# Kernel optimization log

Measured on AMD Instinct MI355X. Metric: run time of the kernel, lower is better.

## Reference

```python
import jax, jax.numpy as jnp
import numpy as np
from jax import lax

B, F, H, W = 1, 8, 16, 16
DIM, HEADS, HD, RANK, T = 1920, 30, 64, 128, 226
SV = F * H * W          # 2048 video tokens
S = T + SV              # 2274 total tokens


def setup_inputs() -> dict:
    key = jax.random.key(0)
    ks = jax.random.split(key, 12)
    r = lambda k, sh, s: jax.random.normal(k, sh, dtype=jnp.float32) * s
    theta = jax.random.uniform(ks[0], (SV, HD), dtype=jnp.float32) * (2.0 * np.pi)
    return dict(
        hidden_states=r(ks[1], (B, SV, DIM), 1.0),
        encoder_hidden_states=r(ks[2], (B, T, DIM), 1.0),
        cos=jnp.cos(theta),
        sin=jnp.sin(theta),
        to_q_w=r(ks[3], (DIM, DIM), 0.02), to_q_b=r(ks[4], (DIM,), 0.02),
        to_k_w=r(ks[5], (DIM, DIM), 0.02), to_k_b=r(ks[6], (DIM,), 0.02),
        to_v_w=r(ks[7], (DIM, DIM), 0.02), to_v_b=r(ks[8], (DIM,), 0.02),
        norm_q_w=jnp.ones((HD,), jnp.float32), norm_q_b=jnp.zeros((HD,), jnp.float32),
        norm_k_w=jnp.ones((HD,), jnp.float32), norm_k_b=jnp.zeros((HD,), jnp.float32),
        conv1_w=r(ks[9], (RANK, DIM, 3), 0.05),
        conv2_w=r(ks[10], (DIM, RANK, 3), 0.05),
        to_out_w=r(ks[11], (DIM, DIM), 0.02),
        to_out_b=jnp.zeros((DIM,), jnp.float32),
    )


def _layernorm(x, w, b, eps=1e-6):
    mu = jnp.mean(x, axis=-1, keepdims=True)
    var = jnp.mean(jnp.square(x - mu), axis=-1, keepdims=True)
    return (x - mu) * lax.rsqrt(var + eps) * w + b


def _rope(x, cos, sin):
    # diffusers interleaved RoPE: pairs (even, odd) along last dim
    xr, xi = x[..., 0::2], x[..., 1::2]
    x_rot = jnp.stack([-xi, xr], axis=-1).reshape(x.shape)
    return x * cos + x_rot * sin


def _conv1d(x, w):  # x: [N, C, L], w: [O, I, K], SAME padding
    return lax.conv_general_dilated(x, w, window_strides=(1,), padding=((1, 1),),
                                    dimension_numbers=('NCH', 'OIH', 'NCH'))


def reference(hidden_states, encoder_hidden_states, cos, sin,
              to_q_w, to_q_b, to_k_w, to_k_b, to_v_w, to_v_b,
              norm_q_w, norm_q_b, norm_k_w, norm_k_b,
              conv1_w, conv2_w, to_out_w, to_out_b):
    # --- temporal conv1d side branch on video tokens only ---
    x = hidden_states.reshape(B, F, H, W, DIM)
    x = jnp.transpose(x, (0, 2, 3, 4, 1)).reshape(B * H * W, DIM, F)  # [BHW, C, F]
    x = _conv1d(x, conv1_w)
    x = jax.nn.gelu(x, approximate=False)
    x = _conv1d(x, conv2_w)
    x = x.reshape(B, H, W, DIM, F)
    conv_branch = jnp.transpose(x, (0, 4, 1, 2, 3)).reshape(B, SV, DIM)

    # --- joint text+video attention ---
    hs = jnp.concatenate([encoder_hidden_states, hidden_states], axis=1)  # [B, S, D]
    q = hs @ to_q_w.T + to_q_b
    k = hs @ to_k_w.T + to_k_b
    v = hs @ to_v_w.T + to_v_b
    q = q.reshape(B, S, HEADS, HD).transpose(0, 2, 1, 3)  # [B, Hh, S, hd]
    k = k.reshape(B, S, HEADS, HD).transpose(0, 2, 1, 3)
    v = v.reshape(B, S, HEADS, HD).transpose(0, 2, 1, 3)

    q = _layernorm(q, norm_q_w, norm_q_b)
    k = _layernorm(k, norm_k_w, norm_k_b)

    # partial RoPE: only video portion (tokens past text_seq_length)
    q = jnp.concatenate([q[:, :, :T], _rope(q[:, :, T:], cos, sin)], axis=2)
    k = jnp.concatenate([k[:, :, :T], _rope(k[:, :, T:], cos, sin)], axis=2)

    scale = 1.0 / np.sqrt(HD).astype(np.float32)
    scores = jnp.einsum('bhqd,bhkd->bhqk', q, k) * scale
    probs = jax.nn.softmax(scores, axis=-1)
    out = jnp.einsum('bhqk,bhkd->bhqd', probs, v)
    out = out.transpose(0, 2, 1, 3).reshape(B, S, DIM)

    # residual add of conv branch into video slice
    out = jnp.concatenate([out[:, :T], out[:, T:] + conv_branch], axis=1)
    out = out @ to_out_w.T + to_out_b

    return out[:, T:], out[:, :T]  # (hidden_states, encoder_hidden_states)
```

## Files before the change

### kernel.cpp

```cpp
#include <hip/hip_runtime.h>
#include <hip/hip_bf16.h>
#include <math.h>

#define F_     8
#define DIM_   1920
#define HEADS_ 30
#define HD_    64
#define RANK_  128
#define T_     226
#define SV_    2048
#define S_     2274

#define BM 128
#define BN 128
#define BK 32

using short8  = __attribute__((ext_vector_type(8))) short;
using f32x4   = __attribute__((ext_vector_type(4))) float;
using i32x4v  = __attribute__((ext_vector_type(4))) int;
using ushort4v= __attribute__((ext_vector_type(4))) unsigned short;

__device__ __forceinline__ unsigned short f2b(float f) {
  unsigned int u = __float_as_uint(f);
  u = (u + 0x7FFFu + ((u >> 16) & 1u)) >> 16;
  return (unsigned short)u;
}
__device__ __forceinline__ float b2f(unsigned short s) {
  return __uint_as_float(((unsigned int)s) << 16);
}
__device__ __forceinline__ void gload_lds16(const void* g, void* l) {
  __builtin_amdgcn_global_load_lds(
      (const __attribute__((address_space(1))) unsigned int*)g,
      (__attribute__((address_space(3))) unsigned int*)l, 16, 0, 0);
}
__device__ __forceinline__ void xcd_swz(int& bx, int& by) {
  const int nx = gridDim.x;
  const int nwg = nx * gridDim.y;
  const int lid = by * nx + bx;
  const int q = nwg >> 3, r = nwg & 7;
  const int xcd = lid & 7, pos = lid >> 3;
  const int wg = (xcd < r ? xcd * (q + 1) : r * (q + 1) + (xcd - r) * q) + pos;
  bx = wg % nx; by = wg / nx;
}

template<int AMODE, int OUTMODE>
__global__ __launch_bounds__(256) void gemm_mfma(
    const unsigned short* __restrict__ A,
    const unsigned short* __restrict__ A2,
    const unsigned short* __restrict__ B,
    const float* __restrict__ bias,
    void* __restrict__ Cout,
    int M, int N, int K, int lda, int ldb, int kinner)
{
  __shared__ __align__(16) unsigned short As[BM * BK];
  __shared__ __align__(16) unsigned short Bs[BN * BK];
  if constexpr (AMODE == 3) {
    const int z = blockIdx.z;
    A += (size_t)z * 480;
    B += (size_t)(z >> 2) * 256 * DIM_ + (z & 3) * 480;
    Cout = (void*)((float*)Cout + (size_t)z * M * N);
  }
  int bx = blockIdx.x, by = blockIdx.y;
  xcd_swz(bx, by);
  const int t   = threadIdx.x;
  const int w   = t >> 6, l = t & 63;
  const int wr  = w >> 1, wc = w & 1;
  const int row0 = by * BM, col0 = bx * BN;
  const int lr  = l & 15;
  const int lcg = l >> 4;
  const int sel = (lr >> 1) & 3;
  const int sr  = t >> 2;
  const int sc  = t & 3;

  f32x4 acc[4][4];
#pragma unroll
  for (int i = 0; i < 4; ++i)
#pragma unroll
    for (int j = 0; j < 4; ++j) acc[i][j] = (f32x4){0.f, 0.f, 0.f, 0.f};

  for (int k0 = 0; k0 < K; k0 += BK) {
    int kseg = 0, kcol = k0;
    if constexpr (AMODE == 1) { kseg = k0 / kinner; kcol = k0 - kseg * kinner; }
#pragma unroll
    for (int it = 0; it < 2; ++it) {
      const int r    = it * 64 + sr;
      const int csrc = sc ^ ((r >> 1) & 3);
      int ar = row0 + r; if (ar > M - 1) ar = M - 1;
      const unsigned short* asrc;
      if constexpr (AMODE == 1) {
        asrc = A + (size_t)(ar + kseg * 256) * kinner + kcol + csrc * 8;
      } else if constexpr (AMODE == 2) {
        asrc = (ar < T_) ? (A  + (size_t)ar        * DIM_ + k0 + csrc * 8)
                         : (A2 + (size_t)(ar - T_) * DIM_ + k0 + csrc * 8);
      } else {
        asrc = A + (size_t)ar * lda + k0 + csrc * 8;
      }
      gload_lds16(asrc, (char*)As + it * 4096 + t * 16);
      const unsigned short* bsrc = B + (size_t)(col0 + r) * ldb + k0 + csrc * 8;
      gload_lds16(bsrc, (char*)Bs + it * 4096 + t * 16);
    }
    __syncthreads();

    short8 af[4], bfv[4];
#pragma unroll
    for (int m = 0; m < 4; ++m) {
      int r = wr * 64 + m * 16 + lr;
      af[m] = *(const short8*)((const char*)As + r * 64 + ((lcg ^ sel) << 4));
    }
#pragma unroll
    for (int n = 0; n < 4; ++n) {
      int r = wc * 64 + n * 16 + lr;
      bfv[n] = *(const short8*)((const char*)Bs + r * 64 + ((lcg ^ sel) << 4));
    }
    __builtin_amdgcn_s_setprio(1);
#pragma unroll
    for (int m = 0; m < 4; ++m)
#pragma unroll
      for (int n = 0; n < 4; ++n)
        acc[m][n] = __builtin_amdgcn_mfma_f32_16x16x32_bf16(af[m], bfv[n], acc[m][n], 0, 0, 0);
    __builtin_amdgcn_s_setprio(0);
    __syncthreads();
  }

#pragma unroll
  for (int m = 0; m < 4; ++m) {
    const int rbase = row0 + wr * 64 + m * 16 + lcg * 4;
#pragma unroll
    for (int n = 0; n < 4; ++n) {
      const int c = col0 + wc * 64 + n * 16 + lr;
      const float bi = bias ? bias[c] : 0.f;
#pragma unroll
      for (int reg = 0; reg < 4; ++reg) {
        const int r = rbase + reg;
        if (r >= M) continue;
        const float v = acc[m][n][reg] + bi;
        if constexpr (OUTMODE == 0) {
          ((float*)Cout)[(size_t)r * N + c] = v;
        } else if constexpr (OUTMODE == 1) {
          ((unsigned short*)Cout)[(size_t)r * N + c] = f2b(v);
        } else if constexpr (OUTMODE == 2) {
          const size_t orow = (r >= T_) ? (size_t)(r - T_) : (size_t)(SV_ + r);
          ((float*)Cout)[orow * N + c] = v;
        } else {
          const int buf = c / DIM_, cc = c - buf * DIM_;
          ((unsigned short*)Cout)[(size_t)buf * S_ * DIM_ + (size_t)r * DIM_ + cc] = f2b(v);
        }
      }
    }
  }
}

__global__ __launch_bounds__(256) void attn_mfma(
    const unsigned short* __restrict__ Qbb,
    const unsigned short* __restrict__ Kbb,
    const unsigned short* __restrict__ Vbb,
    unsigned short* __restrict__ Op0,
    unsigned short* __restrict__ Op1,
    float* __restrict__ ml)
{
  __shared__ __align__(16) unsigned short Kl[2][64 * 64];
  __shared__ __align__(16) unsigned short Vt[2][64 * 64];

  const int sv = blockIdx.z;
  int bx = blockIdx.x, by = blockIdx.y;
  xcd_swz(bx, by);
  const int qb = bx, h = by;
  const int t = threadIdx.x, w = t >> 6, l = t & 63;
  const int lr = l & 15, lg = l >> 4;
  const int q0 = qb * 64;
  const int j0base = sv * 1152;
  const int NT = 18;
  unsigned short* Opart = sv ? Op1 : Op0;

  short8 qa[2];
  {
    int qrow = q0 + w * 16 + lr; if (qrow >= S_) qrow = S_ - 1;
    const unsigned short* qp = Qbb + (size_t)qrow * DIM_ + h * 64 + lg * 8;
    qa[0] = *(const short8*)qp;
    qa[1] = *(const short8*)(qp + 32);
  }

  const int krow0 = t >> 3;
  const int kc0 = ((((t & 7) * 16) ^ ((krow0        & 7) << 4)) >> 1);
  const int kc1 = ((((t & 7) * 16) ^ (((krow0 + 32) & 7) << 4)) >> 1);

  f32x4 oacc[4];
#pragma unroll
  for (int n = 0; n < 4; ++n) oacc[n] = (f32x4){0.f, 0.f, 0.f, 0.f};
  float m_run = -1e30f, l_run = 0.f;

  const int addrA = (lr + ((lg & 1) << 5)) << 2;
  const bool hi_m = (lg & 2) != 0;

  {
    int k0 = j0base + krow0;      if (k0 >= S_) k0 = S_ - 1;
    int k1 = j0base + krow0 + 32; if (k1 >= S_) k1 = S_ - 1;
    gload_lds16(Kbb + (size_t)k0 * DIM_ + h * 64 + kc0, (char*)Kl[0] + t * 16);
    gload_lds16(Kbb + (size_t)k1 * DIM_ + h * 64 + kc1, (char*)Kl[0] + 4096 + t * 16);
    int key = j0base + l; if (key >= S_) key = S_ - 1;
    const unsigned short* vp = Vbb + (size_t)key * DIM_ + h * 64 + w * 16;
    short8 v0 = *(const short8*)vp;
    short8 v1 = *(const short8*)(vp + 8);
#pragma unroll
    for (int i = 0; i < 8; ++i)
      Vt[0][(w * 16 + i) * 64 + (l ^ ((i & 7) << 3))] = (unsigned short)v0[i];
#pragma unroll
    for (int i = 8; i < 16; ++i)
      Vt[0][(w * 16 + i) * 64 + (l ^ ((i & 7) << 3))] = (unsigned short)v1[i - 8];
  }
  __syncthreads();

  for (int jt = 0; jt < NT; ++jt) {
    const int j0 = j0base + jt * 64;
    const int cur = jt & 1;

    const int jn0 = (jt + 1 < NT) ? j0 + 64 : j0;
    {
      int k0 = jn0 + krow0;      if (k0 >= S_) k0 = S_ - 1;
      int k1 = jn0 + krow0 + 32; if (k1 >= S_) k1 = S_ - 1;
      gload_lds16(Kbb + (size_t)k0 * DIM_ + h * 64 + kc0,
                  (char*)Kl[cur ^ 1] + t * 16);
      gload_lds16(Kbb + (size_t)k1 * DIM_ + h * 64 + kc1,
                  (char*)Kl[cur ^ 1] + 4096 + t * 16);
    }
    short8 nv0, nv1;
    {
      int key = jn0 + l; if (key >= S_) key = S_ - 1;
      const unsigned short* vp = Vbb + (size_t)key * DIM_ + h * 64 + w * 16;
      nv0 = *(const short8*)vp;
      nv1 = *(const short8*)(vp + 8);
    }

    f32x4 sacc[4];
#pragma unroll
    for (int m = 0; m < 4; ++m) sacc[m] = (f32x4){0.f, 0.f, 0.f, 0.f};
    __builtin_amdgcn_s_setprio(1);
#pragma unroll
    for (int m = 0; m < 4; ++m) {
#pragma unroll
      for (int ks = 0; ks < 2; ++ks) {
        const short8 kb = *(const short8*)((const char*)Kl[cur] + (m * 16 + lr) * 128 +
                              ((ks * 64 + lg * 16) ^ ((lr & 7) << 4)));
        sacc[m] = __builtin_amdgcn_mfma_f32_16x16x32_bf16(kb, qa[ks], sacc[m], 0, 0, 0);
      }
    }
    __builtin_amdgcn_s_setprio(0);
    if (j0 + 64 > S_) {
#pragma unroll
      for (int m = 0; m < 4; ++m)
#pragma unroll
        for (int r = 0; r < 4; ++r)
          if (j0 + m * 16 + lg * 4 + r >= S_) sacc[m][r] = -1e30f;
    }

    float mx = sacc[0][0];
#pragma unroll
    for (int m = 0; m < 4; ++m)
#pragma unroll
      for (int r = 0; r < 4; ++r) mx = fmaxf(mx, sacc[m][r]);
    mx = fmaxf(mx, __shfl_xor(mx, 16));
    mx = fmaxf(mx, __shfl_xor(mx, 32));

    if (!__all(mx <= m_run + 8.0f)) {
      const float mnew = fmaxf(m_run, mx);
      const float sc = exp2f(m_run - mnew);
      l_run *= sc;
      float scr[4];
#pragma unroll
      for (int r = 0; r < 4; ++r) scr[r] = __shfl(sc, (l & 48) | (lg * 4 + r));
#pragma unroll
      for (int n = 0; n < 4; ++n)
#pragma unroll
        for (int r = 0; r < 4; ++r) oacc[n][r] *= scr[r];
      m_run = mnew;
    }

    float rs = 0.f;
    int c[4][2];
#pragma unroll
    for (int m = 0; m < 4; ++m) {
      const float p0 = exp2f(sacc[m][0] - m_run);
      const float p1 = exp2f(sacc[m][1] - m_run);
      const float p2 = exp2f(sacc[m][2] - m_run);
      const float p3 = exp2f(sacc[m][3] - m_run);
      rs += (p0 + p1) + (p2 + p3);
      asm("v_cvt_pk_bf16_f32 %0, %1, %2" : "=v"(c[m][0]) : "v"(p0), "v"(p1));
      asm("v_cvt_pk_bf16_f32 %0, %1, %2" : "=v"(c[m][1]) : "v"(p2), "v"(p3));
    }
    rs += __shfl_xor(rs, 16);
    rs += __shfl_xor(rs, 32);
    l_run += rs;

    __builtin_amdgcn_s_setprio(1);
#pragma unroll
    for (int ks = 0; ks < 2; ++ks) {
      const int a0 = __builtin_amdgcn_ds_bpermute(addrA,      c[2 * ks][0]);
      const int b0 = __builtin_amdgcn_ds_bpermute(addrA,      c[2 * ks + 1][0]);
      const int a1 = __builtin_amdgcn_ds_bpermute(addrA,      c[2 * ks][1]);
      const int b1 = __builtin_amdgcn_ds_bpermute(addrA,      c[2 * ks + 1][1]);
      const int a2 = __builtin_amdgcn_ds_bpermute(addrA + 64, c[2 * ks][0]);
      const int b2 = __builtin_amdgcn_ds_bpermute(addrA + 64, c[2 * ks + 1][0]);
      const int a3 = __builtin_amdgcn_ds_bpermute(addrA + 64, c[2 * ks][1]);
      const int b3 = __builtin_amdgcn_ds_bpermute(addrA + 64, c[2 * ks + 1][1]);
      i32x4v pw;
      pw[0] = hi_m ? b0 : a0;
      pw[1] = hi_m ? b1 : a1;
      pw[2] = hi_m ? b2 : a2;
      pw[3] = hi_m ? b3 : a3;
      const short8 pa = __builtin_bit_cast(short8, pw);
#pragma unroll
      for (int n = 0; n < 4; ++n) {
        const short8 vb = *(const short8*)((const char*)Vt[cur] + (n * 16 + lr) * 128 +
                              ((ks * 64 + lg * 16) ^ ((lr & 7) << 4)));
        oacc[n] = __builtin_amdgcn_mfma_f32_16x16x32_bf16(pa, vb, oacc[n], 0, 0, 0);
      }
    }
    __builtin_amdgcn_s_setprio(0);

#pragma unroll
    for (int i = 0; i < 8; ++i)
      Vt[cur ^ 1][(w * 16 + i) * 64 + (l ^ ((i & 7) << 3))] = (unsigned short)nv0[i];
#pragma unroll
    for (int i = 8; i < 16; ++i)
      Vt[cur ^ 1][(w * 16 + i) * 64 + (l ^ ((i & 7) << 3))] = (unsigned short)nv1[i - 8];
    __syncthreads();
  }

#pragma unroll
  for (int r = 0; r < 4; ++r) {
    const int row = q0 + w * 16 + lg * 4 + r;
    if (row >= S_) continue;
#pragma unroll
    for (int n = 0; n < 4; ++n)
      Opart[(size_t)row * DIM_ + h * 64 + n * 16 + lr] = f2b(oacc[n][r]);
  }
  if (l < 16) {
    const int row = q0 + w * 16 + lr;
    if (row < S_) {
      float2 v; v.x = m_run; v.y = l_run;
      *(float2*)(ml + ((size_t)(sv * S_ + row) * HEADS_ + h) * 2) = v;
    }
  }
}

__global__ void merge_k(const unsigned short* __restrict__ Op0,
                        const unsigned short* __restrict__ Op1,
                        const float* __restrict__ ml,
                        const unsigned short* __restrict__ y2b,
                        unsigned short* __restrict__ dst)
{
  const int i = blockIdx.x * 256 + threadIdx.x;
  if (i >= S_ * DIM_ / 8) return;
  const int e = i * 8;
  const int row = e / DIM_, col = e % DIM_;
  const int h = col >> 6;
  const float* p0 = ml + ((size_t)row * HEADS_ + h) * 2;
  const float* p1 = ml + ((size_t)(S_ + row) * HEADS_ + h) * 2;
  const float m0 = p0[0], l0 = p0[1], m1 = p1[0], l1 = p1[1];
  const float M = fmaxf(m0, m1);
  const float w0 = exp2f(m0 - M), w1 = exp2f(m1 - M);
  const float inv = 1.f / (w0 * l0 + w1 * l1);
  const short8 a = *(const short8*)(Op0 + e);
  const short8 b = *(const short8*)(Op1 + e);
  const bool cadd = row >= T_;
  const unsigned short* yp = y2b + (size_t)(row - T_) * DIM_ + col;
  short8 o;
#pragma unroll
  for (int j = 0; j < 8; ++j) {
    float v = (w0 * b2f((unsigned short)a[j]) + w1 * b2f((unsigned short)b[j])) * inv;
    if (cadd) v += b2f(yp[j]);
    o[j] = (short)f2b(v);
  }
  *(short8*)(dst + e) = o;
}

#define U0_ 1228800
#define U1_ 3993600
#define U2_ 4427520
#define U3_ 5164800
#define U4_ 5902080
#define U5_ 5907840
__global__ void prep_all(const float* __restrict__ hid, const float* __restrict__ enc,
                         const float* __restrict__ w1, const float* __restrict__ w2,
                         const float* __restrict__ qw, const float* __restrict__ kw,
                         const float* __restrict__ vw, const float* __restrict__ qb2,
                         const float* __restrict__ kb2, const float* __restrict__ vb2,
                         unsigned short* __restrict__ hidpad, unsigned short* __restrict__ encb,
                         unsigned short* __restrict__ w1p, unsigned short* __restrict__ w2p,
                         unsigned short* __restrict__ wqkv, float* __restrict__ bqkv)
{
  const int i = blockIdx.x * 256 + threadIdx.x;
  if (i < U0_) {
    const int e = i * 4;
    const int r = e / DIM_;
    ushort4v o = (ushort4v){0, 0, 0, 0};
    if (r >= 256 && r < 256 + SV_) {
      const float4 v = *(const float4*)(hid + e - 256 * DIM_);
      o[0] = f2b(v.x); o[1] = f2b(v.y); o[2] = f2b(v.z); o[3] = f2b(v.w);
    }
    *(ushort4v*)(hidpad + e) = o;
  } else if (i < U1_) {
    const int e = (i - U0_) * 4;
    const int which = e / (DIM_ * DIM_);
    const int j = e - which * DIM_ * DIM_;
    const float* s = which == 0 ? qw : which == 1 ? kw : vw;
    const float4 v = *(const float4*)(s + j);
    ushort4v o = {f2b(v.x), f2b(v.y), f2b(v.z), f2b(v.w)};
    *(ushort4v*)(wqkv + e) = o;
  } else if (i < U2_) {
    const int e = i - U1_;
    encb[e] = f2b(enc[e]);
  } else if (i < U3_) {
    const int e = i - U2_;
    const int oc = e / (DIM_ * 3), rem = e % (DIM_ * 3);
    const int ks = rem / DIM_, ic = rem % DIM_;
    w1p[e] = f2b(w1[(size_t)oc * DIM_ * 3 + ic * 3 + ks]);
  } else if (i < U4_) {
    const int e = i - U3_;
    const int oc = e / (RANK_ * 3), rem = e % (RANK_ * 3);
    const int ks = rem / RANK_, rc = rem % RANK_;
    w2p[e] = f2b(w2[(size_t)oc * RANK_ * 3 + rc * 3 + ks]);
  } else if (i < U5_) {
    const int e = i - U4_;
    const int which = e / DIM_, j = e % DIM_;
    bqkv[e] = which == 0 ? qb2[j] : which == 1 ? kb2[j] : vb2[j];
  }
}

__global__ void cvt_w(const float* __restrict__ src, unsigned short* __restrict__ dst, int n)
{
  int i = blockIdx.x * 256 + threadIdx.x;
  if (i < n) dst[i] = f2b(src[i]);
}

__global__ void gelupad_k(const float* __restrict__ y1T, unsigned short* __restrict__ dst)
{
  int i = blockIdx.x * 256 + threadIdx.x;
  if (i >= 2560 * RANK_) return;
  int r = i / RANK_, rc = i % RANK_;
  unsigned short o = 0;
  if (r >= 256 && r < 256 + SV_) {
    int s = r - 256;
    float x = 0.f;
#pragma unroll
    for (int z = 0; z < 12; ++z)
      x += y1T[(size_t)z * RANK_ * SV_ + (size_t)rc * SV_ + s];
    o = f2b(0.5f * x * (1.f + erff(x * 0.70710678118654752f)));
  }
  dst[i] = o;
}

__global__ __launch_bounds__(256) void qknorm_rope(
    unsigned short* __restrict__ Qbb, unsigned short* __restrict__ Kbb,
    const float* __restrict__ nq_w, const float* __restrict__ nq_b,
    const float* __restrict__ nk_w, const float* __restrict__ nk_b,
    const float* __restrict__ cosT, const float* __restrict__ sinT)
{
  const int w = threadIdx.x >> 6, lane = threadIdx.x & 63;
  const int idx = blockIdx.x * 4 + w;
  if (idx >= S_ * HEADS_) return;
  const int s = idx / HEADS_, h = idx % HEADS_;
  unsigned short* X = blockIdx.y ? Kbb : Qbb;
  const float* wt = blockIdx.y ? nk_w : nq_w;
  const float* bt = blockIdx.y ? nk_b : nq_b;
  const size_t off = (size_t)s * DIM_ + h * HD_ + lane;
  float x = b2f(X[off]);
  float m = x;
#pragma unroll
  for (int o = 32; o; o >>= 1) m += __shfl_xor(m, o);
  m *= (1.f / 64.f);
  float d = x - m;
  float v = d * d;
#pragma unroll
  for (int o = 32; o; o >>= 1) v += __shfl_xor(v, o);
  v *= (1.f / 64.f);
  float y = d * rsqrtf(v + 1e-6f) * wt[lane] + bt[lane];
  if (s >= T_) {
    float p = __shfl_xor(y, 1);
    float rot = (lane & 1) ? p : -p;
    int sv = s - T_;
    y = y * cosT[(size_t)sv * HD_ + lane] + rot * sinT[(size_t)sv * HD_ + lane];
  }
  if (!blockIdx.y) y *= 0.18033688011112042f;
  X[off] = f2b(y);
}

extern "C" void kernel_launch(void* const* d_in, const int* in_sizes, int n_in,
                              void* d_out, int out_size, void* d_ws, size_t ws_size,
                              hipStream_t stream)
{
  const float* hidden  = (const float*)d_in[0];
  const float* encoder = (const float*)d_in[1];
  const float* cosT    = (const float*)d_in[2];
  const float* sinT    = (const float*)d_in[3];
  const float* to_q_w  = (const float*)d_in[4];
  const float* to_q_b  = (const float*)d_in[5];
  const float* to_k_w  = (const float*)d_in[6];
  const float* to_k_b  = (const float*)d_in[7];
  const float* to_v_w  = (const float*)d_in[8];
  const float* to_v_b  = (const float*)d_in[9];
  const float* nq_w    = (const float*)d_in[10];
  const float* nq_b    = (const float*)d_in[11];
  const float* nk_w    = (const float*)d_in[12];
  const float* nk_b    = (const float*)d_in[13];
  const float* conv1_w = (const float*)d_in[14];
  const float* conv2_w = (const float*)d_in[15];
  const float* to_out_w = (const float*)d_in[16];
  const float* to_out_b = (const float*)d_in[17];
  float* out = (float*)d_out;

  char* p = (char*)d_ws;
  unsigned short* hidpad = (unsigned short*)p;  p += (size_t)2560 * DIM_ * 2;
  unsigned short* y2b    = (unsigned short*)p;  p += (size_t)SV_ * DIM_ * 2;
  unsigned short* wqkv   = (unsigned short*)p;  p += (size_t)3 * DIM_ * DIM_ * 2;
  unsigned short* w1p    = (unsigned short*)p;  p += (size_t)RANK_ * DIM_ * 3 * 2;
  unsigned short* w2p    = (unsigned short*)p;  p += (size_t)DIM_ * RANK_ * 3 * 2;
  unsigned short* QKVbb  = (unsigned short*)p;  p += (size_t)3 * S_ * DIM_ * 2;
  unsigned short* encb   = (unsigned short*)p;  p += (size_t)T_ * DIM_ * 2;
  float*          y1T    = (float*)p;           p += (size_t)12 * RANK_ * SV_ * 4;
  unsigned short* gelup  = (unsigned short*)p;  p += (size_t)2560 * RANK_ * 2;
  float*          bqkv   = (float*)p;           p += (size_t)3 * DIM_ * 4;
  unsigned short* Qbb = QKVbb;
  unsigned short* Kbb = QKVbb + (size_t)S_ * DIM_;
  unsigned short* Vbb = QKVbb + (size_t)2 * S_ * DIM_;
  unsigned short* Op0 = hidpad;
  unsigned short* Op1 = (unsigned short*)y1T;
  float*          ml  = (float*)((char*)y1T + (size_t)S_ * DIM_ * 2);

  prep_all<<<(U5_ + 255) / 256, 256, 0, stream>>>(
      hidden, encoder, conv1_w, conv2_w, to_q_w, to_k_w, to_v_w,
      to_q_b, to_k_b, to_v_b, hidpad, encb, w1p, w2p, wqkv, bqkv);

  gemm_mfma<3, 0><<<dim3(SV_ / BN, 1, 12), 256, 0, stream>>>(
      w1p, nullptr, hidpad, nullptr, y1T, RANK_, SV_, 480, DIM_ * 3, DIM_, 1);
  gelupad_k<<<(2560 * RANK_ + 255) / 256, 256, 0, stream>>>(y1T, gelup);
  gemm_mfma<1, 1><<<dim3(DIM_ / BN, SV_ / BM), 256, 0, stream>>>(
      gelup, nullptr, w2p, nullptr, y2b, SV_, DIM_, RANK_ * 3, RANK_ * 3, RANK_ * 3, RANK_);

  const unsigned short* hid0 = hidpad + (size_t)256 * DIM_;
  gemm_mfma<2, 3><<<dim3(3 * DIM_ / BN, (S_ + BM - 1) / BM), 256, 0, stream>>>(
      encb, hid0, wqkv, bqkv, QKVbb, S_, 3 * DIM_, DIM_, DIM_, DIM_, 1);

  qknorm_rope<<<dim3((S_ * HEADS_ + 3) / 4, 2), 256, 0, stream>>>(
      Qbb, Kbb, nq_w, nq_b, nk_w, nk_b, cosT, sinT);

  attn_mfma<<<dim3((S_ + 63) / 64, HEADS_, 2), 256, 0, stream>>>(
      Qbb, Kbb, Vbb, Op0, Op1, ml);

  merge_k<<<(S_ * DIM_ / 8 + 255) / 256, 256, 0, stream>>>(Op0, Op1, ml, y2b, Qbb);

  cvt_w<<<(DIM_ * DIM_ + 255) / 256, 256, 0, stream>>>(to_out_w, wqkv, DIM_ * DIM_);
  gemm_mfma<0, 2><<<dim3(DIM_ / BN, (S_ + BM - 1) / BM), 256, 0, stream>>>(
      Qbb, nullptr, wqkv, to_out_b, out, S_, DIM_, DIM_, DIM_, DIM_, 1);
}
```

Measured before the change: 406.2 us.

## Process two query tiles per wave in attention and fuse out-weight cast into merge

Each attention wave now handles 32 query rows as two 16-row sub-tiles that share every K and V tile loaded from shared memory. This halves the grid, the K/V global and LDS traffic per query, and the loop overhead. The to_out weight bf16 conversion is folded into the merge kernel with vectorised loads, removing one launch. The trade-offs are more registers per thread, possibly lower occupancy, and fewer blocks (18×30×2) to fill the GPU.

```diff
diff --git a/kernel.cpp b/kernel.cpp
--- a/kernel.cpp
+++ b/kernel.cpp
@@ -150,6 +150,24 @@
   }
 }
 
+__device__ __forceinline__ short8 build_pa(int c0lo, int c0hi, int c1lo, int c1hi,
+                                           int addrA, bool hi_m) {
+  const int a0 = __builtin_amdgcn_ds_bpermute(addrA,      c0lo);
+  const int b0 = __builtin_amdgcn_ds_bpermute(addrA,      c1lo);
+  const int a1 = __builtin_amdgcn_ds_bpermute(addrA,      c0hi);
+  const int b1 = __builtin_amdgcn_ds_bpermute(addrA,      c1hi);
+  const int a2 = __builtin_amdgcn_ds_bpermute(addrA + 64, c0lo);
+  const int b2 = __builtin_amdgcn_ds_bpermute(addrA + 64, c1lo);
+  const int a3 = __builtin_amdgcn_ds_bpermute(addrA + 64, c0hi);
+  const int b3 = __builtin_amdgcn_ds_bpermute(addrA + 64, c1hi);
+  i32x4v pw;
+  pw[0] = hi_m ? b0 : a0;
+  pw[1] = hi_m ? b1 : a1;
+  pw[2] = hi_m ? b2 : a2;
+  pw[3] = hi_m ? b3 : a3;
+  return __builtin_bit_cast(short8, pw);
+}
+
 __global__ __launch_bounds__(256) void attn_mfma(
     const unsigned short* __restrict__ Qbb,
     const unsigned short* __restrict__ Kbb,
@@ -167,27 +185,32 @@
   const int qb = bx, h = by;
   const int t = threadIdx.x, w = t >> 6, l = t & 63;
   const int lr = l & 15, lg = l >> 4;
-  const int q0 = qb * 64;
+  const int q0 = qb * 128;
   const int j0base = sv * 1152;
   const int NT = 18;
   unsigned short* Opart = sv ? Op1 : Op0;
 
-  short8 qa[2];
+  short8 qaA[2], qaB[2];
   {
-    int qrow = q0 + w * 16 + lr; if (qrow >= S_) qrow = S_ - 1;
-    const unsigned short* qp = Qbb + (size_t)qrow * DIM_ + h * 64 + lg * 8;
-    qa[0] = *(const short8*)qp;
-    qa[1] = *(const short8*)(qp + 32);
+    int qrA = q0 + w * 32 + lr;      if (qrA >= S_) qrA = S_ - 1;
+    int qrB = q0 + w * 32 + 16 + lr; if (qrB >= S_) qrB = S_ - 1;
+    const unsigned short* qpA = Qbb + (size_t)qrA * DIM_ + h * 64 + lg * 8;
+    const unsigned short* qpB = Qbb + (size_t)qrB * DIM_ + h * 64 + lg * 8;
+    qaA[0] = *(const short8*)qpA; qaA[1] = *(const short8*)(qpA + 32);
+    qaB[0] = *(const short8*)qpB; qaB[1] = *(const short8*)(qpB + 32);
   }
 
   const int krow0 = t >> 3;
   const int kc0 = ((((t & 7) * 16) ^ ((krow0        & 7) << 4)) >> 1);
   const int kc1 = ((((t & 7) * 16) ^ (((krow0 + 32) & 7) << 4)) >> 1);
 
-  f32x4 oacc[4];
-#pragma unroll
-  for (int n = 0; n < 4; ++n) oacc[n] = (f32x4){0.f, 0.f, 0.f, 0.f};
-  float m_run = -1e30f, l_run = 0.f;
+  f32x4 oaccA[4], oaccB[4];
+#pragma unroll
+  for (int n = 0; n < 4; ++n) {
+    oaccA[n] = (f32x4){0.f, 0.f, 0.f, 0.f};
+    oaccB[n] = (f32x4){0.f, 0.f, 0.f, 0.f};
+  }
+  float mA = -1e30f, lA = 0.f, mB = -1e30f, lB = 0.f;
 
   const int addrA = (lr + ((lg & 1) << 5)) << 2;
   const bool hi_m = (lg & 2) != 0;
@@ -231,9 +254,9 @@
       nv1 = *(const short8*)(vp + 8);
     }
 
-    f32x4 sacc[4];
-#pragma unroll
-    for (int m = 0; m < 4; ++m) sacc[m] = (f32x4){0.f, 0.f, 0.f, 0.f};
+    f32x4 sA[4], sB[4];
+#pragma unroll
+    for (int m = 0; m < 4; ++m) { sA[m] = (f32x4){0.f,0.f,0.f,0.f}; sB[m] = (f32x4){0.f,0.f,0.f,0.f}; }
     __builtin_amdgcn_s_setprio(1);
 #pragma unroll
     for (int m = 0; m < 4; ++m) {
@@ -241,7 +264,8 @@
       for (int ks = 0; ks < 2; ++ks) {
         const short8 kb = *(const short8*)((const char*)Kl[cur] + (m * 16 + lr) * 128 +
                               ((ks * 64 + lg * 16) ^ ((lr & 7) << 4)));
-        sacc[m] = __builtin_amdgcn_mfma_f32_16x16x32_bf16(kb, qa[ks], sacc[m], 0, 0, 0);
+        sA[m] = __builtin_amdgcn_mfma_f32_16x16x32_bf16(kb, qaA[ks], sA[m], 0, 0, 0);
+        sB[m] = __builtin_amdgcn_mfma_f32_16x16x32_bf16(kb, qaB[ks], sB[m], 0, 0, 0);
       }
     }
     __builtin_amdgcn_s_setprio(0);
@@ -250,69 +274,65 @@
       for (int m = 0; m < 4; ++m)
 #pragma unroll
         for (int r = 0; r < 4; ++r)
-          if (j0 + m * 16 + lg * 4 + r >= S_) sacc[m][r] = -1e30f;
-    }
-
-    float mx = sacc[0][0];
+          if (j0 + m * 16 + lg * 4 + r >= S_) { sA[m][r] = -1e30f; sB[m][r] = -1e30f; }
+    }
+
+    float mxA = sA[0][0], mxB = sB[0][0];
 #pragma unroll
     for (int m = 0; m < 4; ++m)
 #pragma unroll
-      for (int r = 0; r < 4; ++r) mx = fmaxf(mx, sacc[m][r]);
-    mx = fmaxf(mx, __shfl_xor(mx, 16));
-    mx = fmaxf(mx, __shfl_xor(mx, 32));
-
-    if (!__all(mx <= m_run + 8.0f)) {
-      const float mnew = fmaxf(m_run, mx);
-      const float sc = exp2f(m_run - mnew);
-      l_run *= sc;
-      float scr[4];
-#pragma unroll
-      for (int r = 0; r < 4; ++r) scr[r] = __shfl(sc, (l & 48) | (lg * 4 + r));
+      for (int r = 0; r < 4; ++r) { mxA = fmaxf(mxA, sA[m][r]); mxB = fmaxf(mxB, sB[m][r]); }
+    mxA = fmaxf(mxA, __shfl_xor(mxA, 16));
+    mxA = fmaxf(mxA, __shfl_xor(mxA, 32));
+    mxB = fmaxf(mxB, __shfl_xor(mxB, 16));
+    mxB = fmaxf(mxB, __shfl_xor(mxB, 32));
+
+    if (!__all(mxA <= mA + 8.0f && mxB <= mB + 8.0f)) {
+      const float mnA = fmaxf(mA, mxA), mnB = fmaxf(mB, mxB);
+      const float scA = exp2f(mA - mnA), scB = exp2f(mB - mnB);
+      lA *= scA; lB *= scB;
+      float srA[4], srB[4];
+#pragma unroll
+      for (int r = 0; r < 4; ++r) {
+        srA[r] = __shfl(scA, (l & 48) | (lg * 4 + r));
+        srB[r] = __shfl(scB, (l & 48) | (lg * 4 + r));
+      }
 #pragma unroll
       for (int n = 0; n < 4; ++n)
 #pragma unroll
-        for (int r = 0; r < 4; ++r) oacc[n][r] *= scr[r];
-      m_run = mnew;
-    }
-
-    float rs = 0.f;
-    int c[4][2];
+        for (int r = 0; r < 4; ++r) { oaccA[n][r] *= srA[r]; oaccB[n][r] *= srB[r]; }
+      mA = mnA; mB = mnB;
+    }
+
+    float rsA = 0.f, rsB = 0.f;
+    int cA[4][2], cB[4][2];
 #pragma unroll
     for (int m = 0; m < 4; ++m) {
-      const float p0 = exp2f(sacc[m][0] - m_run);
-      const float p1 = exp2f(sacc[m][1] - m_run);
-      const float p2 = exp2f(sacc[m][2] - m_run);
-      const float p3 = exp2f(sacc[m][3] - m_run);
-      rs += (p0 + p1) + (p2 + p3);
-      asm("v_cvt_pk_bf16_f32 %0, %1, %2" : "=v"(c[m][0]) : "v"(p0), "v"(p1));
-      asm("v_cvt_pk_bf16_f32 %0, %1, %2" : "=v"(c[m][1]) : "v"(p2), "v"(p3));
-    }
-    rs += __shfl_xor(rs, 16);
-    rs += __shfl_xor(rs, 32);
-    l_run += rs;
+      const float a0 = exp2f(sA[m][0] - mA), a1 = exp2f(sA[m][1] - mA);
+      const float a2 = exp2f(sA[m][2] - mA), a3 = exp2f(sA[m][3] - mA);
+      rsA += (a0 + a1) + (a2 + a3);
+      asm("v_cvt_pk_bf16_f32 %0, %1, %2" : "=v"(cA[m][0]) : "v"(a0), "v"(a1));
+      asm("v_cvt_pk_bf16_f32 %0, %1, %2" : "=v"(cA[m][1]) : "v"(a2), "v"(a3));
+      const float b0 = exp2f(sB[m][0] - mB), b1 = exp2f(sB[m][1] - mB);
+      const float b2 = exp2f(sB[m][2] - mB), b3 = exp2f(sB[m][3] - mB);
+      rsB += (b0 + b1) + (b2 + b3);
+      asm("v_cvt_pk_bf16_f32 %0, %1, %2" : "=v"(cB[m][0]) : "v"(b0), "v"(b1));
+      asm("v_cvt_pk_bf16_f32 %0, %1, %2" : "=v"(cB[m][1]) : "v"(b2), "v"(b3));
+    }
+    rsA += __shfl_xor(rsA, 16); rsA += __shfl_xor(rsA, 32); lA += rsA;
+    rsB += __shfl_xor(rsB, 16); rsB += __shfl_xor(rsB, 32); lB += rsB;
 
     __builtin_amdgcn_s_setprio(1);
 #pragma unroll
     for (int ks = 0; ks < 2; ++ks) {
-      const int a0 = __builtin_amdgcn_ds_bpermute(addrA,      c[2 * ks][0]);
-      const int b0 = __builtin_amdgcn_ds_bpermute(addrA,      c[2 * ks + 1][0]);
-      const int a1 = __builtin_amdgcn_ds_bpermute(addrA,      c[2 * ks][1]);
-      const int b1 = __builtin_amdgcn_ds_bpermute(addrA,      c[2 * ks + 1][1]);
-      const int a2 = __builtin_amdgcn_ds_bpermute(addrA + 64, c[2 * ks][0]);
-      const int b2 = __builtin_amdgcn_ds_bpermute(addrA + 64, c[2 * ks + 1][0]);
-      const int a3 = __builtin_amdgcn_ds_bpermute(addrA + 64, c[2 * ks][1]);
-      const int b3 = __builtin_amdgcn_ds_bpermute(addrA + 64, c[2 * ks + 1][1]);
-      i32x4v pw;
-      pw[0] = hi_m ? b0 : a0;
-      pw[1] = hi_m ? b1 : a1;
-      pw[2] = hi_m ? b2 : a2;
-      pw[3] = hi_m ? b3 : a3;
-      const short8 pa = __builtin_bit_cast(short8, pw);
+      const short8 paA = build_pa(cA[2*ks][0], cA[2*ks][1], cA[2*ks+1][0], cA[2*ks+1][1], addrA, hi_m);
+      const short8 paB = build_pa(cB[2*ks][0], cB[2*ks][1], cB[2*ks+1][0], cB[2*ks+1][1], addrA, hi_m);
 #pragma unroll
       for (int n = 0; n < 4; ++n) {
         const short8 vb = *(const short8*)((const char*)Vt[cur] + (n * 16 + lr) * 128 +
                               ((ks * 64 + lg * 16) ^ ((lr & 7) << 4)));
-        oacc[n] = __builtin_amdgcn_mfma_f32_16x16x32_bf16(pa, vb, oacc[n], 0, 0, 0);
+        oaccA[n] = __builtin_amdgcn_mfma_f32_16x16x32_bf16(paA, vb, oaccA[n], 0, 0, 0);
+        oaccB[n] = __builtin_amdgcn_mfma_f32_16x16x32_bf16(paB, vb, oaccB[n], 0, 0, 0);
       }
     }
     __builtin_amdgcn_s_setprio(0);
@@ -328,50 +348,75 @@
 
 #pragma unroll
   for (int r = 0; r < 4; ++r) {
-    const int row = q0 + w * 16 + lg * 4 + r;
-    if (row >= S_) continue;
-#pragma unroll
-    for (int n = 0; n < 4; ++n)
-      Opart[(size_t)row * DIM_ + h * 64 + n * 16 + lr] = f2b(oacc[n][r]);
+    const int rowA = q0 + w * 32 + lg * 4 + r;
+    const int rowB = rowA + 16;
+    if (rowA < S_) {
+#pragma unroll
+      for (int n = 0; n < 4; ++n)
+        Opart[(size_t)rowA * DIM_ + h * 64 + n * 16 + lr] = f2b(oaccA[n][r]);
+    }
+    if (rowB < S_) {
+#pragma unroll
+      for (int n = 0; n < 4; ++n)
+        Opart[(size_t)rowB * DIM_ + h * 64 + n * 16 + lr] = f2b(oaccB[n][r]);
+    }
   }
   if (l < 16) {
-    const int row = q0 + w * 16 + lr;
-    if (row < S_) {
-      float2 v; v.x = m_run; v.y = l_run;
-      *(float2*)(ml + ((size_t)(sv * S_ + row) * HEADS_ + h) * 2) = v;
-    }
-  }
-}
-
+    const int rowA = q0 + w * 32 + lr;
+    const int rowB = rowA + 16;
+    if (rowA < S_) {
+      float2 v; v.x = mA; v.y = lA;
+      *(float2*)(ml + ((size_t)(sv * S_ + rowA) * HEADS_ + h) * 2) = v;
+    }
+    if (rowB < S_) {
+      float2 v; v.x = mB; v.y = lB;
+      *(float2*)(ml + ((size_t)(sv * S_ + rowB) * HEADS_ + h) * 2) = v;
+    }
+  }
+}
+
+#define MERGE_N_ (S_ * DIM_ / 8)
+#define CVT_N_   (DIM_ * DIM_ / 8)
 __global__ void merge_k(const unsigned short* __restrict__ Op0,
                         const unsigned short* __restrict__ Op1,
                         const float* __restrict__ ml,
                         const unsigned short* __restrict__ y2b,
-                        unsigned short* __restrict__ dst)
+                        unsigned short* __restrict__ dst,
+                        const float* __restrict__ ow,
+                        unsigned short* __restrict__ owb)
 {
   const int i = blockIdx.x * 256 + threadIdx.x;
-  if (i >= S_ * DIM_ / 8) return;
-  const int e = i * 8;
-  const int row = e / DIM_, col = e % DIM_;
-  const int h = col >> 6;
-  const float* p0 = ml + ((size_t)row * HEADS_ + h) * 2;
-  const float* p1 = ml + ((size_t)(S_ + row) * HEADS_ + h) * 2;
-  const float m0 = p0[0], l0 = p0[1], m1 = p1[0], l1 = p1[1];
-  const float M = fmaxf(m0, m1);
-  const float w0 = exp2f(m0 - M), w1 = exp2f(m1 - M);
-  const float inv = 1.f / (w0 * l0 + w1 * l1);
-  const short8 a = *(const short8*)(Op0 + e);
-  const short8 b = *(const short8*)(Op1 + e);
-  const bool cadd = row >= T_;
-  const unsigned short* yp = y2b + (size_t)(row - T_) * DIM_ + col;
-  short8 o;
-#pragma unroll
-  for (int j = 0; j < 8; ++j) {
-    float v = (w0 * b2f((unsigned short)a[j]) + w1 * b2f((unsigned short)b[j])) * inv;
-    if (cadd) v += b2f(yp[j]);
-    o[j] = (short)f2b(v);
-  }
-  *(short8*)(dst + e) = o;
+  if (i < MERGE_N_) {
+    const int e = i * 8;
+    const int row = e / DIM_, col = e % DIM_;
+    const int h = col >> 6;
+    const float* p0 = ml + ((size_t)row * HEADS_ + h) * 2;
+    const float* p1 = ml + ((size_t)(S_ + row) * HEADS_ + h) * 2;
+    const float m0 = p0[0], l0 = p0[1], m1 = p1[0], l1 = p1[1];
+    const float M = fmaxf(m0, m1);
+    const float w0 = exp2f(m0 - M), w1 = exp2f(m1 - M);
+    const float inv = 1.f / (w0 * l0 + w1 * l1);
+    const short8 a = *(const short8*)(Op0 + e);
+    const short8 b = *(const short8*)(Op1 + e);
+    const bool cadd = row >= T_;
+    const unsigned short* yp = y2b + (size_t)(row - T_) * DIM_ + col;
+    short8 o;
+#pragma unroll
+    for (int j = 0; j < 8; ++j) {
+      float v = (w0 * b2f((unsigned short)a[j]) + w1 * b2f((unsigned short)b[j])) * inv;
+      if (cadd) v += b2f(yp[j]);
+      o[j] = (short)f2b(v);
+    }
+    *(short8*)(dst + e) = o;
+  } else if (i < MERGE_N_ + CVT_N_) {
+    const int e = (i - MERGE_N_) * 8;
+    const float4 v0 = *(const float4*)(ow + e);
+    const float4 v1 = *(const float4*)(ow + e + 4);
+    short8 o;
+    o[0]=(short)f2b(v0.x); o[1]=(short)f2b(v0.y); o[2]=(short)f2b(v0.z); o[3]=(short)f2b(v0.w);
+    o[4]=(short)f2b(v1.x); o[5]=(short)f2b(v1.y); o[6]=(short)f2b(v1.z); o[7]=(short)f2b(v1.w);
+    *(short8*)(owb + e) = o;
+  }
 }
 
 #define U0_ 1228800
@@ -427,12 +472,6 @@
   }
 }
 
-__global__ void cvt_w(const float* __restrict__ src, unsigned short* __restrict__ dst, int n)
-{
-  int i = blockIdx.x * 256 + threadIdx.x;
-  if (i < n) dst[i] = f2b(src[i]);
-}
-
 __global__ void gelupad_k(const float* __restrict__ y1T, unsigned short* __restrict__ dst)
 {
   int i = blockIdx.x * 256 + threadIdx.x;
@@ -544,12 +583,12 @@
   qknorm_rope<<<dim3((S_ * HEADS_ + 3) / 4, 2), 256, 0, stream>>>(
       Qbb, Kbb, nq_w, nq_b, nk_w, nk_b, cosT, sinT);
 
-  attn_mfma<<<dim3((S_ + 63) / 64, HEADS_, 2), 256, 0, stream>>>(
+  attn_mfma<<<dim3((S_ + 127) / 128, HEADS_, 2), 256, 0, stream>>>(
       Qbb, Kbb, Vbb, Op0, Op1, ml);
 
-  merge_k<<<(S_ * DIM_ / 8 + 255) / 256, 256, 0, stream>>>(Op0, Op1, ml, y2b, Qbb);
-
-  cvt_w<<<(DIM_ * DIM_ + 255) / 256, 256, 0, stream>>>(to_out_w, wqkv, DIM_ * DIM_);
+  merge_k<<<(MERGE_N_ + CVT_N_ + 255) / 256, 256, 0, stream>>>(
+      Op0, Op1, ml, y2b, Qbb, to_out_w, wqkv);
+
   gemm_mfma<0, 2><<<dim3(DIM_ / BN, (S_ + BM - 1) / BM), 256, 0, stream>>>(
       Qbb, nullptr, wqkv, to_out_b, out, S_, DIM_, DIM_, DIM_, DIM_, 1);
 }
```

Result: slower. 420.2 us (+3.4%).

## Write V transposed from QKV GEMM and feed attention PV directly from global

Applied to the files above, without the earlier changes.

The QKV projection epilogue now writes the V third as a transposed [DIM, padded-S] bf16 buffer using 4-wide stores. The attention kernel then loads V^T fragments straight into registers, split across the QK^T phase. This removes the per-tile LDS transpose, its scalar shared-memory writes and half the LDS footprint. Separately, the to_out weight conversion is folded into the merge kernel with vectorized loads, saving one launch. The trade-offs are strided, less-coalesced GEMM epilogue stores and global-latency V reads inside the attention loop. The padding columns of V^T are never initialized, so stale or NaN values there could leak into the output even though the matching probabilities are zero.

```diff
diff --git a/kernel.cpp b/kernel.cpp
--- a/kernel.cpp
+++ b/kernel.cpp
@@ -10,6 +10,7 @@
 #define T_     226
 #define SV_    2048
 #define S_     2274
+#define SP_    2304
 
 #define BM 128
 #define BN 128
@@ -50,6 +51,7 @@
     const unsigned short* __restrict__ B,
     const float* __restrict__ bias,
     void* __restrict__ Cout,
+    unsigned short* __restrict__ VT,
     int M, int N, int K, int lda, int ldb, int kinner)
 {
   __shared__ __align__(16) unsigned short As[BM * BK];
@@ -129,37 +131,75 @@
     for (int n = 0; n < 4; ++n) {
       const int c = col0 + wc * 64 + n * 16 + lr;
       const float bi = bias ? bias[c] : 0.f;
-#pragma unroll
-      for (int reg = 0; reg < 4; ++reg) {
-        const int r = rbase + reg;
-        if (r >= M) continue;
-        const float v = acc[m][n][reg] + bi;
-        if constexpr (OUTMODE == 0) {
-          ((float*)Cout)[(size_t)r * N + c] = v;
-        } else if constexpr (OUTMODE == 1) {
-          ((unsigned short*)Cout)[(size_t)r * N + c] = f2b(v);
-        } else if constexpr (OUTMODE == 2) {
-          const size_t orow = (r >= T_) ? (size_t)(r - T_) : (size_t)(SV_ + r);
-          ((float*)Cout)[orow * N + c] = v;
+      if constexpr (OUTMODE == 3) {
+        const int buf = c / DIM_, cc = c - buf * DIM_;
+        if (buf == 2) {
+          unsigned short* vt = VT + (size_t)cc * SP_ + rbase;
+          if (rbase + 4 <= M) {
+            ushort4v o = {f2b(acc[m][n][0] + bi), f2b(acc[m][n][1] + bi),
+                          f2b(acc[m][n][2] + bi), f2b(acc[m][n][3] + bi)};
+            *(ushort4v*)vt = o;
+          } else {
+#pragma unroll
+            for (int reg = 0; reg < 4; ++reg)
+              if (rbase + reg < M) vt[reg] = f2b(acc[m][n][reg] + bi);
+          }
         } else {
-          const int buf = c / DIM_, cc = c - buf * DIM_;
-          ((unsigned short*)Cout)[(size_t)buf * S_ * DIM_ + (size_t)r * DIM_ + cc] = f2b(v);
+#pragma unroll
+          for (int reg = 0; reg < 4; ++reg) {
+            const int r = rbase + reg;
+            if (r < M)
+              ((unsigned short*)Cout)[(size_t)buf * S_ * DIM_ + (size_t)r * DIM_ + cc]
+                  = f2b(acc[m][n][reg] + bi);
+          }
+        }
+      } else {
+#pragma unroll
+        for (int reg = 0; reg < 4; ++reg) {
+          const int r = rbase + reg;
+          if (r >= M) continue;
+          const float v = acc[m][n][reg] + bi;
+          if constexpr (OUTMODE == 0) {
+            ((float*)Cout)[(size_t)r * N + c] = v;
+          } else if constexpr (OUTMODE == 1) {
+            ((unsigned short*)Cout)[(size_t)r * N + c] = f2b(v);
+          } else {
+            const size_t orow = (r >= T_) ? (size_t)(r - T_) : (size_t)(SV_ + r);
+            ((float*)Cout)[orow * N + c] = v;
+          }
         }
       }
     }
   }
+}
+
+__device__ __forceinline__ short8 build_pa(int c0lo, int c0hi, int c1lo, int c1hi,
+                                           int addrA, bool hi_m) {
+  const int a0 = __builtin_amdgcn_ds_bpermute(addrA,      c0lo);
+  const int b0 = __builtin_amdgcn_ds_bpermute(addrA,      c1lo);
+  const int a1 = __builtin_amdgcn_ds_bpermute(addrA,      c0hi);
+  const int b1 = __builtin_amdgcn_ds_bpermute(addrA,      c1hi);
+  const int a2 = __builtin_amdgcn_ds_bpermute(addrA + 64, c0lo);
+  const int b2 = __builtin_amdgcn_ds_bpermute(addrA + 64, c1lo);
+  const int a3 = __builtin_amdgcn_ds_bpermute(addrA + 64, c0hi);
+  const int b3 = __builtin_amdgcn_ds_bpermute(addrA + 64, c1hi);
+  i32x4v pw;
+  pw[0] = hi_m ? b0 : a0;
+  pw[1] = hi_m ? b1 : a1;
+  pw[2] = hi_m ? b2 : a2;
+  pw[3] = hi_m ? b3 : a3;
+  return __builtin_bit_cast(short8, pw);
 }
 
 __global__ __launch_bounds__(256) void attn_mfma(
     const unsigned short* __restrict__ Qbb,
     const unsigned short* __restrict__ Kbb,
-    const unsigned short* __restrict__ Vbb,
+    const unsigned short* __restrict__ VT,
     unsigned short* __restrict__ Op0,
     unsigned short* __restrict__ Op1,
     float* __restrict__ ml)
 {
   __shared__ __align__(16) unsigned short Kl[2][64 * 64];
-  __shared__ __align__(16) unsigned short Vt[2][64 * 64];
 
   const int sv = blockIdx.z;
   int bx = blockIdx.x, by = blockIdx.y;
@@ -179,6 +219,7 @@
     qa[0] = *(const short8*)qp;
     qa[1] = *(const short8*)(qp + 32);
   }
+  const unsigned short* vtb = VT + (size_t)(h * 64 + lr) * SP_ + lg * 8;
 
   const int krow0 = t >> 3;
   const int kc0 = ((((t & 7) * 16) ^ ((krow0        & 7) << 4)) >> 1);
@@ -197,16 +238,6 @@
     int k1 = j0base + krow0 + 32; if (k1 >= S_) k1 = S_ - 1;
     gload_lds16(Kbb + (size_t)k0 * DIM_ + h * 64 + kc0, (char*)Kl[0] + t * 16);
     gload_lds16(Kbb + (size_t)k1 * DIM_ + h * 64 + kc1, (char*)Kl[0] + 4096 + t * 16);
-    int key = j0base + l; if (key >= S_) key = S_ - 1;
-    const unsigned short* vp = Vbb + (size_t)key * DIM_ + h * 64 + w * 16;
-    short8 v0 = *(const short8*)vp;
-    short8 v1 = *(const short8*)(vp + 8);
-#pragma unroll
-    for (int i = 0; i < 8; ++i)
-      Vt[0][(w * 16 + i) * 64 + (l ^ ((i & 7) << 3))] = (unsigned short)v0[i];
-#pragma unroll
-    for (int i = 8; i < 16; ++i)
-      Vt[0][(w * 16 + i) * 64 + (l ^ ((i & 7) << 3))] = (unsigned short)v1[i - 8];
   }
   __syncthreads();
 
@@ -223,13 +254,11 @@
       gload_lds16(Kbb + (size_t)k1 * DIM_ + h * 64 + kc1,
                   (char*)Kl[cur ^ 1] + 4096 + t * 16);
     }
-    short8 nv0, nv1;
-    {
-      int key = jn0 + l; if (key >= S_) key = S_ - 1;
-      const unsigned short* vp = Vbb + (size_t)key * DIM_ + h * 64 + w * 16;
-      nv0 = *(const short8*)vp;
-      nv1 = *(const short8*)(vp + 8);
-    }
+
+    short8 vb0[4], vb1[4];
+#pragma unroll
+    for (int n = 0; n < 4; ++n)
+      vb0[n] = *(const short8*)(vtb + (size_t)(n * 16) * SP_ + j0);
 
     f32x4 sacc[4];
 #pragma unroll
@@ -245,6 +274,10 @@
       }
     }
     __builtin_amdgcn_s_setprio(0);
+#pragma unroll
+    for (int n = 0; n < 4; ++n)
+      vb1[n] = *(const short8*)(vtb + (size_t)(n * 16) * SP_ + j0 + 32);
+
     if (j0 + 64 > S_) {
 #pragma unroll
       for (int m = 0; m < 4; ++m)
@@ -292,37 +325,18 @@
     l_run += rs;
 
     __builtin_amdgcn_s_setprio(1);
-#pragma unroll
-    for (int ks = 0; ks < 2; ++ks) {
-      const int a0 = __builtin_amdgcn_ds_bpermute(addrA,      c[2 * ks][0]);
-      const int b0 = __builtin_amdgcn_ds_bpermute(addrA,      c[2 * ks + 1][0]);
-      const int a1 = __builtin_amdgcn_ds_bpermute(addrA,      c[2 * ks][1]);
-      const int b1 = __builtin_amdgcn_ds_bpermute(addrA,      c[2 * ks + 1][1]);
-      const int a2 = __builtin_amdgcn_ds_bpermute(addrA + 64, c[2 * ks][0]);
-      const int b2 = __builtin_amdgcn_ds_bpermute(addrA + 64, c[2 * ks + 1][0]);
-      const int a3 = __builtin_amdgcn_ds_bpermute(addrA + 64, c[2 * ks][1]);
-      const int b3 = __builtin_amdgcn_ds_bpermute(addrA + 64, c[2 * ks + 1][1]);
-      i32x4v pw;
-      pw[0] = hi_m ? b0 : a0;
-      pw[1] = hi_m ? b1 : a1;
-      pw[2] = hi_m ? b2 : a2;
-      pw[3] = hi_m ? b3 : a3;
-      const short8 pa = __builtin_bit_cast(short8, pw);
-#pragma unroll
-      for (int n = 0; n < 4; ++n) {
-        const short8 vb = *(const short8*)((const char*)Vt[cur] + (n * 16 + lr) * 128 +
-                              ((ks * 64 + lg * 16) ^ ((lr & 7) << 4)));
-        oacc[n] = __builtin_amdgcn_mfma_f32_16x16x32_bf16(pa, vb, oacc[n], 0, 0, 0);
-      }
+    {
+      const short8 pa0 = build_pa(c[0][0], c[0][1], c[1][0], c[1][1], addrA, hi_m);
+#pragma unroll
+      for (int n = 0; n < 4; ++n)
+        oacc[n] = __builtin_amdgcn_mfma_f32_16x16x32_bf16(pa0, vb0[n], oacc[n], 0, 0, 0);
+      const short8 pa1 = build_pa(c[2][0], c[2][1], c[3][0], c[3][1], addrA, hi_m);
+#pragma unroll
+      for (int n = 0; n < 4; ++n)
+        oacc[n] = __builtin_amdgcn_mfma_f32_16x16x32_bf16(pa1, vb1[n], oacc[n], 0, 0, 0);
     }
     __builtin_amdgcn_s_setprio(0);
 
-#pragma unroll
-    for (int i = 0; i < 8; ++i)
-      Vt[cur ^ 1][(w * 16 + i) * 64 + (l ^ ((i & 7) << 3))] = (unsigned short)nv0[i];
-#pragma unroll
-    for (int i = 8; i < 16; ++i)
-      Vt[cur ^ 1][(w * 16 + i) * 64 + (l ^ ((i & 7) << 3))] = (unsigned short)nv1[i - 8];
     __syncthreads();
   }
 
@@ -343,35 +357,48 @@
   }
 }
 
+#define MERGE_N_ (S_ * DIM_ / 8)
+#define CVT_N_   (DIM_ * DIM_ / 8)
 __global__ void merge_k(const unsigned short* __restrict__ Op0,
                         const unsigned short* __restrict__ Op1,
                         const float* __restrict__ ml,
                         const unsigned short* __restrict__ y2b,
-                        unsigned short* __restrict__ dst)
+                        unsigned short* __restrict__ dst,
+                        const float* __restrict__ ow,
+                        unsigned short* __restrict__ owb)
 {
   const int i = blockIdx.x * 256 + threadIdx.x;
-  if (i >= S_ * DIM_ / 8) return;
-  const int e = i * 8;
-  const int row = e / DIM_, col = e % DIM_;
-  const int h = col >> 6;
-  const float* p0 = ml + ((size_t)row * HEADS_ + h) * 2;
-  const float* p1 = ml + ((size_t)(S_ + row) * HEADS_ + h) * 2;
-  const float m0 = p0[0], l0 = p0[1], m1 = p1[0], l1 = p1[1];
-  const float M = fmaxf(m0, m1);
-  const float w0 = exp2f(m0 - M), w1 = exp2f(m1 - M);
-  const float inv = 1.f / (w0 * l0 + w1 * l1);
-  const short8 a = *(const short8*)(Op0 + e);
-  const short8 b = *(const short8*)(Op1 + e);
-  const bool cadd = row >= T_;
-  const unsigned short* yp = y2b + (size_t)(row - T_) * DIM_ + col;
-  short8 o;
-#pragma unroll
-  for (int j = 0; j < 8; ++j) {
-    float v = (w0 * b2f((unsigned short)a[j]) + w1 * b2f((unsigned short)b[j])) * inv;
-    if (cadd) v += b2f(yp[j]);
-    o[j] = (short)f2b(v);
-  }
-  *(short8*)(dst + e) = o;
+  if (i < MERGE_N_) {
+    const int e = i * 8;
+    const int row = e / DIM_, col = e % DIM_;
+    const int h = col >> 6;
+    const float* p0 = ml + ((size_t)row * HEADS_ + h) * 2;
+    const float* p1 = ml + ((size_t)(S_ + row) * HEADS_ + h) * 2;
+    const float m0 = p0[0], l0 = p0[1], m1 = p1[0], l1 = p1[1];
+    const float M = fmaxf(m0, m1);
+    const float w0 = exp2f(m0 - M), w1 = exp2f(m1 - M);
+    const float inv = 1.f / (w0 * l0 + w1 * l1);
+    const short8 a = *(const short8*)(Op0 + e);
+    const short8 b = *(const short8*)(Op1 + e);
+    const bool cadd = row >= T_;
+    const unsigned short* yp = y2b + (size_t)(row - T_) * DIM_ + col;
+    short8 o;
+#pragma unroll
+    for (int j = 0; j < 8; ++j) {
+      float v = (w0 * b2f((unsigned short)a[j]) + w1 * b2f((unsigned short)b[j])) * inv;
+      if (cadd) v += b2f(yp[j]);
+      o[j] = (short)f2b(v);
+    }
+    *(short8*)(dst + e) = o;
+  } else if (i < MERGE_N_ + CVT_N_) {
+    const int e = (i - MERGE_N_) * 8;
+    const float4 v0 = *(const float4*)(ow + e);
+    const float4 v1 = *(const float4*)(ow + e + 4);
+    short8 o;
+    o[0]=(short)f2b(v0.x); o[1]=(short)f2b(v0.y); o[2]=(short)f2b(v0.z); o[3]=(short)f2b(v0.w);
+    o[4]=(short)f2b(v1.x); o[5]=(short)f2b(v1.y); o[6]=(short)f2b(v1.z); o[7]=(short)f2b(v1.w);
+    *(short8*)(owb + e) = o;
+  }
 }
 
 #define U0_ 1228800
@@ -427,12 +454,6 @@
   }
 }
 
-__global__ void cvt_w(const float* __restrict__ src, unsigned short* __restrict__ dst, int n)
-{
-  int i = blockIdx.x * 256 + threadIdx.x;
-  if (i < n) dst[i] = f2b(src[i]);
-}
-
 __global__ void gelupad_k(const float* __restrict__ y1T, unsigned short* __restrict__ dst)
 {
   int i = blockIdx.x * 256 + threadIdx.x;
@@ -515,14 +536,14 @@
   unsigned short* wqkv   = (unsigned short*)p;  p += (size_t)3 * DIM_ * DIM_ * 2;
   unsigned short* w1p    = (unsigned short*)p;  p += (size_t)RANK_ * DIM_ * 3 * 2;
   unsigned short* w2p    = (unsigned short*)p;  p += (size_t)DIM_ * RANK_ * 3 * 2;
-  unsigned short* QKVbb  = (unsigned short*)p;  p += (size_t)3 * S_ * DIM_ * 2;
+  unsigned short* QKbb   = (unsigned short*)p;  p += (size_t)2 * S_ * DIM_ * 2;
+  unsigned short* VbbT   = (unsigned short*)p;  p += (size_t)DIM_ * SP_ * 2;
   unsigned short* encb   = (unsigned short*)p;  p += (size_t)T_ * DIM_ * 2;
   float*          y1T    = (float*)p;           p += (size_t)12 * RANK_ * SV_ * 4;
   unsigned short* gelup  = (unsigned short*)p;  p += (size_t)2560 * RANK_ * 2;
   float*          bqkv   = (float*)p;           p += (size_t)3 * DIM_ * 4;
-  unsigned short* Qbb = QKVbb;
-  unsigned short* Kbb = QKVbb + (size_t)S_ * DIM_;
-  unsigned short* Vbb = QKVbb + (size_t)2 * S_ * DIM_;
+  unsigned short* Qbb = QKbb;
+  unsigned short* Kbb = QKbb + (size_t)S_ * DIM_;
   unsigned short* Op0 = hidpad;
   unsigned short* Op1 = (unsigned short*)y1T;
   float*          ml  = (float*)((char*)y1T + (size_t)S_ * DIM_ * 2);
@@ -532,24 +553,24 @@
       to_q_b, to_k_b, to_v_b, hidpad, encb, w1p, w2p, wqkv, bqkv);
 
   gemm_mfma<3, 0><<<dim3(SV_ / BN, 1, 12), 256, 0, stream>>>(
-      w1p, nullptr, hidpad, nullptr, y1T, RANK_, SV_, 480, DIM_ * 3, DIM_, 1);
+      w1p, nullptr, hidpad, nullptr, y1T, nullptr, RANK_, SV_, 480, DIM_ * 3, DIM_, 1);
   gelupad_k<<<(2560 * RANK_ + 255) / 256, 256, 0, stream>>>(y1T, gelup);
   gemm_mfma<1, 1><<<dim3(DIM_ / BN, SV_ / BM), 256, 0, stream>>>(
-      gelup, nullptr, w2p, nullptr, y2b, SV_, DIM_, RANK_ * 3, RANK_ * 3, RANK_ * 3, RANK_);
+      gelup, nullptr, w2p, nullptr, y2b, nullptr, SV_, DIM_, RANK_ * 3, RANK_ * 3, RANK_ * 3, RANK_);
 
   const unsigned short* hid0 = hidpad + (size_t)256 * DIM_;
   gemm_mfma<2, 3><<<dim3(3 * DIM_ / BN, (S_ + BM - 1) / BM), 256, 0, stream>>>(
-      encb, hid0, wqkv, bqkv, QKVbb, S_, 3 * DIM_, DIM_, DIM_, DIM_, 1);
+      encb, hid0, wqkv, bqkv, QKbb, VbbT, S_, 3 * DIM_, DIM_, DIM_, DIM_, 1);
 
   qknorm_rope<<<dim3((S_ * HEADS_ + 3) / 4, 2), 256, 0, stream>>>(
       Qbb, Kbb, nq_w, nq_b, nk_w, nk_b, cosT, sinT);
 
   attn_mfma<<<dim3((S_ + 63) / 64, HEADS_, 2), 256, 0, stream>>>(
-      Qbb, Kbb, Vbb, Op0, Op1, ml);
-
-  merge_k<<<(S_ * DIM_ / 8 + 255) / 256, 256, 0, stream>>>(Op0, Op1, ml, y2b, Qbb);
-
-  cvt_w<<<(DIM_ * DIM_ + 255) / 256, 256, 0, stream>>>(to_out_w, wqkv, DIM_ * DIM_);
+      Qbb, Kbb, VbbT, Op0, Op1, ml);
+
+  merge_k<<<(MERGE_N_ + CVT_N_ + 255) / 256, 256, 0, stream>>>(
+      Op0, Op1, ml, y2b, Qbb, to_out_w, wqkv);
+
   gemm_mfma<0, 2><<<dim3(DIM_ / BN, (S_ + BM - 1) / BM), 256, 0, stream>>>(
-      Qbb, nullptr, wqkv, to_out_b, out, S_, DIM_, DIM_, DIM_, DIM_, 1);
-}
+      Qbb, nullptr, wqkv, to_out_b, out, nullptr, S_, DIM_, DIM_, DIM_, DIM_, 1);
+}
```

New measurement: 438.6 us. 1.08x slower.
